# Kernel tuning notes

Measured on AMD Instinct MI355X. Metric: run time of the kernel, lower is better.

The kernel has to match this reference:

```python
import jax, jax.numpy as jnp
import numpy as np

NUM_HEADS = 2
LN_EPS = 1e-5
NEG_MASK = -1e9


def setup_inputs() -> dict:
    key = jax.random.key(0)
    ks = jax.random.split(key, 8)
    B, C, T, N = 8, 64, 32, 400
    H, D = NUM_HEADS, C // NUM_HEADS
    s = 1.0 / np.sqrt(C)
    return {
        "x": jax.random.normal(ks[0], (B, C, T, N), dtype=jnp.float32),
        "Wq": jax.random.normal(ks[1], (C, C), dtype=jnp.float32) * s,
        "Wk": jax.random.normal(ks[2], (C, C), dtype=jnp.float32) * s,
        "Wv": jax.random.normal(ks[3], (C, C), dtype=jnp.float32) * s,
        "a_src": jax.random.normal(ks[4], (H, D), dtype=jnp.float32) * 0.1,
        "a_dst": jax.random.normal(ks[5], (H, D), dtype=jnp.float32) * 0.1,
        "ln_gamma": jnp.ones((C,), dtype=jnp.float32),
        "ln_beta": jnp.zeros((C,), dtype=jnp.float32),
        "gso": jax.random.randint(ks[6], (N, N), 0, 2, dtype=jnp.int32),
    }


def reference(x, Wq, Wk, Wv, a_src, a_dst, ln_gamma, ln_beta, gso):
    B, C, T, N = x.shape
    H = NUM_HEADS
    D = C // H
    # (B,C,T,N) -> (B*T, N, C)
    xr = jnp.transpose(x, (0, 2, 3, 1)).reshape(B * T, N, C)
    # torch Linear: y = x @ W.T; then split heads -> (BT, N, H, D)
    Q = (xr @ Wq.T).reshape(B * T, N, H, D)
    K = (xr @ Wk.T).reshape(B * T, N, H, D)
    V = (xr @ Wv.T).reshape(B * T, N, H, D)
    # GAT additive scores per head
    s_src = jnp.einsum("bnhd,hd->bnh", Q, a_src)  # (BT, N, H)
    s_dst = jnp.einsum("bnhd,hd->bnh", K, a_dst)  # (BT, N, H)
    scores = s_src[:, :, None, :] + s_dst[:, None, :, :]  # (BT, i, j, H)
    scores = jax.nn.leaky_relu(scores, negative_slope=0.2)
    mask = jnp.where(gso == 0, jnp.float32(NEG_MASK), 0.0)  # (N, N)
    scores = scores + mask[None, :, :, None]
    attn = jax.nn.softmax(scores, axis=2)  # softmax over dst j; dropout = identity (eval)
    out = jnp.einsum("bijh,bjhd->bihd", attn, V).reshape(B * T, N, C)
    # LayerNorm over channel dim
    mu = jnp.mean(out, axis=-1, keepdims=True)
    var = jnp.var(out, axis=-1, keepdims=True)
    out = (out - mu) * jax.lax.rsqrt(var + LN_EPS) * ln_gamma + ln_beta
    # (BT, N, C) -> (B, C, T, N)
    return jnp.transpose(out.reshape(B, T, N, C), (0, 3, 1, 2))
```

## Files before the change

### kernel.cpp

```cpp
#include <hip/hip_runtime.h>
#include <hip/hip_bf16.h>

typedef __attribute__((ext_vector_type(8))) short bf16x8;
typedef __attribute__((ext_vector_type(4))) float f32x4;
typedef __attribute__((ext_vector_type(4))) int i32x4;
typedef __attribute__((ext_vector_type(4))) unsigned int u32x4;

#define B_   8
#define C_   64
#define T_   32
#define N_   400
#define BT_  256
#define NCH_ 7
#define NKT_ 13
#define L2E_ 1.4426950408889634f
#define C2_  (-13.849872392533959f)
#define SH12_ (-17.312340490667560f)

#define WS_MB 0
#define WS_SQ 25600
#define WS_SK 844800
#define WS_VG 1664000

#if __has_builtin(__builtin_amdgcn_exp2f)
#define EXP2F(x) __builtin_amdgcn_exp2f(x)
#else
#define EXP2F(x) __expf((x) * 0.6931471805599453f)
#endif

__global__ __launch_bounds__(256, 4) void gat_proj(
    const float* __restrict__ x, const float* __restrict__ Wq,
    const float* __restrict__ Wk, const float* __restrict__ Wv,
    const float* __restrict__ a_src, const float* __restrict__ a_dst,
    const int* __restrict__ gso,
    float* __restrict__ sq1, float* __restrict__ sk1,
    __hip_bfloat16* __restrict__ Vg, unsigned int* __restrict__ mb)
{
  __shared__ __align__(16) float xs[64][65];
  __shared__ __align__(16) float wv_s[64][68];
  __shared__ float wqk_s[4][64];
  const int tid = threadIdx.x;
  const int bt = blockIdx.x & 255, nc = blockIdx.x >> 8;
  const int b = bt >> 5, t = bt & 31, n0 = nc * 64;
  const int w = tid >> 6, nn = tid & 63;

  {
    const int h = w >> 1;
    const float* W = (w & 1) ? Wk : Wq;
    const float* a = (w & 1) ? a_dst : a_src;
    float s = 0.f;
    #pragma unroll
    for (int d = 0; d < 32; ++d)
      s += W[(h*32 + d)*C_ + nn] * a[h*32 + d];
    wqk_s[w][nn] = s;
  }
  #pragma unroll
  for (int it = 0; it < 16; ++it) {
    int idx = it*256 + tid;
    int o = idx >> 6, c = idx & 63;
    wv_s[c][o] = Wv[o*C_ + c];
  }
  #pragma unroll
  for (int it = 0; it < 16; ++it) {
    int idx = it*256 + tid;
    int c = idx >> 6, n2 = idx & 63;
    int n = n0 + n2;
    xs[c][n2] = (n < N_) ? x[((b*C_ + c)*T_ + t)*N_ + n] : 0.f;
  }
  __syncthreads();

  f32x4 a0={0,0,0,0}, a1={0,0,0,0}, a2={0,0,0,0}, a3={0,0,0,0};
  float sacc = 0.f;
  #pragma unroll 4
  for (int c = 0; c < 64; ++c) {
    float xv = xs[c][nn];
    const f32x4* wr = (const f32x4*)&wv_s[c][w*16];
    a0 += xv*wr[0]; a1 += xv*wr[1]; a2 += xv*wr[2]; a3 += xv*wr[3];
    sacc = fmaf(xv, wqk_s[w][c], sacc);
  }
  const int n = n0 + nn;
  if (n < N_) {
    int h = w >> 1;
    if (w & 1) sk1[((size_t)bt*2 + h)*N_ + n] = sacc * L2E_;
    else       sq1[((size_t)bt*2 + h)*N_ + n] = fmaf(sacc, L2E_, SH12_);
  }
  if (n < 416) {
    const int kt = n >> 5, q = (n >> 3) & 3, jj = n & 7;
    __hip_bfloat16* vp = Vg
        + ((((size_t)bt*NKT_ + kt)*2 + (w>>1))*2 + (w&1))*512
        + q*128 + jj;
    #pragma unroll
    for (int k = 0; k < 4; ++k) vp[(0*4+k)*8] = __float2bfloat16(a0[k]);
    #pragma unroll
    for (int k = 0; k < 4; ++k) vp[(1*4+k)*8] = __float2bfloat16(a1[k]);
    #pragma unroll
    for (int k = 0; k < 4; ++k) vp[(2*4+k)*8] = __float2bfloat16(a2[k]);
    #pragma unroll
    for (int k = 0; k < 4; ++k) vp[(3*4+k)*8] = __float2bfloat16(a3[k]);
  }
  if (blockIdx.x < 26) {
    int idx = blockIdx.x*256 + tid;
    if (idx < N_*16) {
      int i = idx >> 4, kw = idx & 15;
      unsigned int bits = 0;
      if (kw < 13) {
        int j0 = kw * 32;
        #pragma unroll
        for (int bb = 0; bb < 32; ++bb) {
          int j = j0 + bb;
          if (j < N_ && gso[i*N_ + j] != 0) bits |= (1u << bb);
        }
      }
      mb[idx] = bits;
    }
  }
}

__global__ __launch_bounds__(512, 6) void gat_attn(
    const __hip_bfloat16* __restrict__ Vg, const float* __restrict__ sq1,
    const float* __restrict__ sk1, const unsigned int* __restrict__ mb,
    const float* __restrict__ gamma, const float* __restrict__ beta,
    float* __restrict__ out)
{
  __shared__ __align__(16) float sd_s[2][416];
  __shared__ __align__(16) float ob[64][65];
  const int tid = threadIdx.x;
  const int bt = blockIdx.x & 255, chunk = blockIdx.x >> 8;
  const int b = bt >> 5, t = bt & 31;
  const int i0 = chunk * 64;

  if (tid < 416) {
    sd_s[0][tid] = (tid < N_) ? sk1[((size_t)bt*2 + 0)*N_ + tid] : 0.f;
    sd_s[1][tid] = (tid < N_) ? sk1[((size_t)bt*2 + 1)*N_ + tid] : 0.f;
  }
  __syncthreads();

  const int lane = tid & 63, wave = tid >> 6;
  const int h = wave & 1, itile = wave >> 1;
  const int rowA = lane & 15, quad = lane >> 4;
  const int ibase = i0 + itile*16;

  if (ibase < N_) {
    const int irow = ibase + rowA;
    const float si1 = sq1[((size_t)bt*2 + h)*N_ + irow];
    const u32x4* mp = (const u32x4*)(mb + irow*16);
    u32x4 mw0 = mp[0], mw1 = mp[1], mw2 = mp[2];
    unsigned int mw12 = mb[irow*16 + 12];
    const float* sdp = sd_s[h] + quad*8;
    const __hip_bfloat16* vbase = Vg + ((size_t)bt*NKT_*2 + h)*2*512 + lane*8;

    f32x4 d0={0,0,0,0}, d1={0,0,0,0}, d2={0,0,0,0};
    bf16x8 ones;
    #pragma unroll
    for (int k = 0; k < 8; ++k) ones[k] = (short)0x3F80;

    #pragma unroll
    for (int kt = 0; kt < NKT_; ++kt) {
      unsigned int mword = (kt < 4) ? mw0[kt] : (kt < 8) ? mw1[kt-4]
                         : (kt < 12) ? mw2[kt-8] : mw12;
      unsigned int mbyte = (mword >> (quad*8)) & 0xffu;
      f32x4 s0 = *(const f32x4*)(sdp + kt*32);
      f32x4 s1 = *(const f32x4*)(sdp + kt*32 + 4);
      bf16x8 vb0 = *(const bf16x8*)(vbase + kt*2048);
      bf16x8 vb1 = *(const bf16x8*)(vbase + kt*2048 + 512);
      int em[8];
      #pragma unroll
      for (int jj = 0; jj < 8; ++jj) {
        float sd = (jj < 4) ? s0[jj] : s1[jj-4];
        float t1 = si1 + sd;
        float t2 = fmaf(0.2f, t1, C2_);
        float v  = fmaxf(t1, t2);
        float e  = EXP2F(v);
        int msk = ((int)(mbyte << (31 - jj))) >> 31;
        em[jj] = __float_as_int(e) & msk;
      }
      union { i32x4 i; bf16x8 v; } af;
      af.i.x = (int)__builtin_amdgcn_perm((unsigned)em[1], (unsigned)em[0], 0x07060302u);
      af.i.y = (int)__builtin_amdgcn_perm((unsigned)em[3], (unsigned)em[2], 0x07060302u);
      af.i.z = (int)__builtin_amdgcn_perm((unsigned)em[5], (unsigned)em[4], 0x07060302u);
      af.i.w = (int)__builtin_amdgcn_perm((unsigned)em[7], (unsigned)em[6], 0x07060302u);
      d0 = __builtin_amdgcn_mfma_f32_16x16x32_bf16(af.v, vb0, d0, 0, 0, 0);
      d1 = __builtin_amdgcn_mfma_f32_16x16x32_bf16(af.v, vb1, d1, 0, 0, 0);
      d2 = __builtin_amdgcn_mfma_f32_16x16x32_bf16(af.v, ones, d2, 0, 0, 0);
    }
    #pragma unroll
    for (int r = 0; r < 4; ++r) {
      float li = 1.0f / d2[r];
      int rl = itile*16 + quad*4 + r;
      ob[rl][h*32 + rowA]      = d0[r] * li;
      ob[rl][h*32 + 16 + rowA] = d1[r] * li;
    }
  }
  __syncthreads();

  {
    int rl = tid >> 3, cgi = tid & 7;
    int n = i0 + rl;
    if (n < N_) {
      float u[8]; float s = 0.f;
      #pragma unroll
      for (int k = 0; k < 8; ++k) { u[k] = ob[rl][cgi*8 + k]; s += u[k]; }
      s += __shfl_xor(s,1); s += __shfl_xor(s,2); s += __shfl_xor(s,4);
      float mu = s * (1.f/64.f);
      float q = 0.f;
      #pragma unroll
      for (int k = 0; k < 8; ++k) { float dv = u[k]-mu; q = fmaf(dv,dv,q); }
      q += __shfl_xor(q,1); q += __shfl_xor(q,2); q += __shfl_xor(q,4);
      float rstd = rsqrtf(q*(1.f/64.f) + 1e-5f);
      #pragma unroll
      for (int k = 0; k < 8; ++k) {
        float g = gamma[cgi*8 + k], be = beta[cgi*8 + k];
        ob[rl][cgi*8 + k] = (u[k]-mu)*rstd*g + be;
      }
    }
  }
  __syncthreads();

  #pragma unroll
  for (int it = 0; it < 8; ++it) {
    int idx = it*512 + tid;
    int c = idx >> 6, nn2 = idx & 63;
    int n = i0 + nn2;
    if (n < N_) out[((b*C_ + c)*T_ + t)*N_ + n] = ob[nn2][c];
  }
}

extern "C" void kernel_launch(void* const* d_in, const int* in_sizes, int n_in,
                              void* d_out, int out_size, void* d_ws, size_t ws_size,
                              hipStream_t stream) {
  (void)in_sizes; (void)n_in; (void)out_size; (void)ws_size;
  const float* x     = (const float*)d_in[0];
  const float* Wq    = (const float*)d_in[1];
  const float* Wk    = (const float*)d_in[2];
  const float* Wv    = (const float*)d_in[3];
  const float* a_src = (const float*)d_in[4];
  const float* a_dst = (const float*)d_in[5];
  const float* gamma = (const float*)d_in[6];
  const float* beta  = (const float*)d_in[7];
  const int*   gso   = (const int*)d_in[8];
  float* out = (float*)d_out;
  char* ws = (char*)d_ws;

  unsigned int* mb = (unsigned int*)(ws + WS_MB);
  float* sq1 = (float*)(ws + WS_SQ);
  float* sk1 = (float*)(ws + WS_SK);
  __hip_bfloat16* Vg = (__hip_bfloat16*)(ws + WS_VG);

  gat_proj<<<BT_*NCH_, 256, 0, stream>>>(x, Wq, Wk, Wv, a_src, a_dst, gso,
                                         sq1, sk1, Vg, mb);
  gat_attn<<<BT_*NCH_, 512, 0, stream>>>(Vg, sq1, sk1, mb,
                                         gamma, beta, out);
}
```

Measured before the change: 134.9 us.

## Fuse projection and attention into one per-timestep block, keeping V in LDS

Replaces the two-kernel pipeline, which wrote scores and bf16 V to global workspace, with one 1024-thread block per (b,t). That block projects V and the scores into shared memory, then runs the masked-softmax MFMA attention plus LayerNorm over row chunks of 128. The mask-bit packing moves to a small separate prep kernel. The goal is to remove the global round trip for V and the scores and the redundant per-chunk reloads. The cost is a grid of only 256 large blocks with around 100KB of LDS each, so occupancy is low and there may be too few blocks to fill the GPU. x is also now rounded to bf16 before projection, which changes precision.

```diff
diff --git a/kernel.cpp b/kernel.cpp
--- a/kernel.cpp
+++ b/kernel.cpp
@@ -3,6 +3,7 @@
 
 typedef __attribute__((ext_vector_type(8))) short bf16x8;
 typedef __attribute__((ext_vector_type(4))) float f32x4;
+typedef __attribute__((ext_vector_type(2))) float f32x2;
 typedef __attribute__((ext_vector_type(4))) int i32x4;
 typedef __attribute__((ext_vector_type(4))) unsigned int u32x4;
 
@@ -11,16 +12,10 @@
 #define T_   32
 #define N_   400
 #define BT_  256
-#define NCH_ 7
 #define NKT_ 13
 #define L2E_ 1.4426950408889634f
 #define C2_  (-13.849872392533959f)
 #define SH12_ (-17.312340490667560f)
-
-#define WS_MB 0
-#define WS_SQ 25600
-#define WS_SK 844800
-#define WS_VG 1664000
 
 #if __has_builtin(__builtin_amdgcn_exp2f)
 #define EXP2F(x) __builtin_amdgcn_exp2f(x)
@@ -28,200 +23,217 @@
 #define EXP2F(x) __expf((x) * 0.6931471805599453f)
 #endif
 
-__global__ __launch_bounds__(256, 4) void gat_proj(
+__global__ __launch_bounds__(256) void gat_prep(
+    const int* __restrict__ gso, unsigned int* __restrict__ mb)
+{
+  int idx = blockIdx.x*256 + threadIdx.x;
+  if (idx < N_*16) {
+    int i = idx >> 4, kw = idx & 15;
+    unsigned int bits = 0;
+    if (kw < 13) {
+      int j0 = kw * 32;
+      #pragma unroll
+      for (int bb = 0; bb < 32; ++bb) {
+        int j = j0 + bb;
+        if (j < N_ && gso[i*N_ + j] != 0) bits |= (1u << bb);
+      }
+    }
+    mb[idx] = bits;
+  }
+}
+
+__global__ __launch_bounds__(1024) void gat_fused(
     const float* __restrict__ x, const float* __restrict__ Wq,
     const float* __restrict__ Wk, const float* __restrict__ Wv,
     const float* __restrict__ a_src, const float* __restrict__ a_dst,
-    const int* __restrict__ gso,
-    float* __restrict__ sq1, float* __restrict__ sk1,
-    __hip_bfloat16* __restrict__ Vg, unsigned int* __restrict__ mb)
+    const float* __restrict__ gamma, const float* __restrict__ beta,
+    const unsigned int* __restrict__ mb, float* __restrict__ out)
 {
-  __shared__ __align__(16) float xs[64][65];
-  __shared__ __align__(16) float wv_s[64][68];
+  __shared__ __align__(16) __hip_bfloat16 Vt[64][416];
+  __shared__ __align__(16) char scratch[70656];
+  __shared__ __align__(16) float sd_s[2][416];
+  __shared__ __align__(16) float si_s[2][400];
   __shared__ float wqk_s[4][64];
+  __shared__ float g_s[64], b_s[64];
+
+  unsigned int (*xs)[208] = (unsigned int(*)[208])scratch;
+  float (*wv_s)[68] = (float(*)[68])(scratch + 53248);
+  float (*ob)[68] = (float(*)[68])scratch;
+
   const int tid = threadIdx.x;
-  const int bt = blockIdx.x & 255, nc = blockIdx.x >> 8;
-  const int b = bt >> 5, t = bt & 31, n0 = nc * 64;
-  const int w = tid >> 6, nn = tid & 63;
-
-  {
-    const int h = w >> 1;
-    const float* W = (w & 1) ? Wk : Wq;
-    const float* a = (w & 1) ? a_dst : a_src;
+  const int bt = blockIdx.x;
+  const int b = bt >> 5, t = bt & 31;
+
+  if (tid < 256) {
+    int ww = tid >> 6, c = tid & 63, h = ww >> 1;
+    const float* W = (ww & 1) ? Wk : Wq;
+    const float* a = (ww & 1) ? a_dst : a_src;
     float s = 0.f;
     #pragma unroll
-    for (int d = 0; d < 32; ++d)
-      s += W[(h*32 + d)*C_ + nn] * a[h*32 + d];
-    wqk_s[w][nn] = s;
+    for (int d = 0; d < 32; ++d) s += W[(h*32 + d)*C_ + c] * a[h*32 + d];
+    wqk_s[ww][c] = s;
+  } else if (tid < 320) {
+    g_s[tid - 256] = gamma[tid - 256];
+  } else if (tid < 384) {
+    b_s[tid - 320] = beta[tid - 320];
+  }
+  #pragma unroll
+  for (int it = 0; it < 4; ++it) {
+    int idx = it*1024 + tid;
+    int o = idx >> 6, c = idx & 63;
+    wv_s[c][o] = Wv[o*C_ + c];
   }
   #pragma unroll
   for (int it = 0; it < 16; ++it) {
-    int idx = it*256 + tid;
-    int o = idx >> 6, c = idx & 63;
-    wv_s[c][o] = Wv[o*C_ + c];
-  }
+    int idx = it*1024 + tid;
+    int c = idx >> 8, pr = idx & 255;
+    if (pr < 208) {
+      int n = pr*2;
+      const float* xrow = x + ((size_t)(b*C_ + c)*T_ + t)*N_;
+      float x0 = (n   < N_) ? xrow[n]   : 0.f;
+      float x1 = (n+1 < N_) ? xrow[n+1] : 0.f;
+      union { __hip_bfloat16 h2[2]; unsigned int u; } pk;
+      pk.h2[0] = __float2bfloat16(x0);
+      pk.h2[1] = __float2bfloat16(x1);
+      xs[c][pr] = pk.u;
+    }
+  }
+  __syncthreads();
+
+  {
+    const int pr = tid >> 2, ww = tid & 3;
+    if (pr < 208) {
+      f32x2 acc[16];
+      #pragma unroll
+      for (int k = 0; k < 16; ++k) acc[k] = (f32x2){0.f, 0.f};
+      f32x2 sacc = {0.f, 0.f};
+      #pragma unroll 4
+      for (int c = 0; c < 64; ++c) {
+        unsigned int xu = xs[c][pr];
+        f32x2 xv;
+        xv.x = __uint_as_float(xu << 16);
+        xv.y = __uint_as_float(xu & 0xffff0000u);
+        const f32x4* wr = (const f32x4*)&wv_s[c][ww*16];
+        f32x4 w0 = wr[0], w1 = wr[1], w2 = wr[2], w3 = wr[3];
+        #pragma unroll
+        for (int k = 0; k < 4; ++k) acc[k]      = xv * w0[k] + acc[k];
+        #pragma unroll
+        for (int k = 0; k < 4; ++k) acc[4 + k]  = xv * w1[k] + acc[4 + k];
+        #pragma unroll
+        for (int k = 0; k < 4; ++k) acc[8 + k]  = xv * w2[k] + acc[8 + k];
+        #pragma unroll
+        for (int k = 0; k < 4; ++k) acc[12 + k] = xv * w3[k] + acc[12 + k];
+        sacc = xv * wqk_s[ww][c] + sacc;
+      }
+      const int n = pr*2, hw = ww >> 1;
+      if (ww & 1) {
+        sd_s[hw][n]   = sacc.x * L2E_;
+        sd_s[hw][n+1] = sacc.y * L2E_;
+      } else {
+        if (n   < N_) si_s[hw][n]   = fmaf(sacc.x, L2E_, SH12_);
+        if (n+1 < N_) si_s[hw][n+1] = fmaf(sacc.y, L2E_, SH12_);
+      }
+      #pragma unroll
+      for (int k = 0; k < 16; ++k) {
+        int o = ww*16 + k;
+        union { __hip_bfloat16 h2[2]; unsigned int u; } pk;
+        pk.h2[0] = __float2bfloat16(acc[k].x);
+        pk.h2[1] = __float2bfloat16(acc[k].y);
+        *(unsigned int*)&Vt[o][n] = pk.u;
+      }
+    }
+  }
+  __syncthreads();
+
+  const int lane = tid & 63, wave = tid >> 6;
+  const int hh = wave & 1, itile = wave >> 1;
+  const int rowA = lane & 15, quad = lane >> 4;
+
+  bf16x8 ones;
   #pragma unroll
-  for (int it = 0; it < 16; ++it) {
-    int idx = it*256 + tid;
-    int c = idx >> 6, n2 = idx & 63;
-    int n = n0 + n2;
-    xs[c][n2] = (n < N_) ? x[((b*C_ + c)*T_ + t)*N_ + n] : 0.f;
-  }
-  __syncthreads();
-
-  f32x4 a0={0,0,0,0}, a1={0,0,0,0}, a2={0,0,0,0}, a3={0,0,0,0};
-  float sacc = 0.f;
-  #pragma unroll 4
-  for (int c = 0; c < 64; ++c) {
-    float xv = xs[c][nn];
-    const f32x4* wr = (const f32x4*)&wv_s[c][w*16];
-    a0 += xv*wr[0]; a1 += xv*wr[1]; a2 += xv*wr[2]; a3 += xv*wr[3];
-    sacc = fmaf(xv, wqk_s[w][c], sacc);
-  }
-  const int n = n0 + nn;
-  if (n < N_) {
-    int h = w >> 1;
-    if (w & 1) sk1[((size_t)bt*2 + h)*N_ + n] = sacc * L2E_;
-    else       sq1[((size_t)bt*2 + h)*N_ + n] = fmaf(sacc, L2E_, SH12_);
-  }
-  if (n < 416) {
-    const int kt = n >> 5, q = (n >> 3) & 3, jj = n & 7;
-    __hip_bfloat16* vp = Vg
-        + ((((size_t)bt*NKT_ + kt)*2 + (w>>1))*2 + (w&1))*512
-        + q*128 + jj;
+  for (int k = 0; k < 8; ++k) ones[k] = (short)0x3F80;
+
+  for (int r0 = 0; r0 < N_; r0 += 128) {
+    const int ibase = r0 + itile*16;
+    if (ibase < N_) {
+      const int irow = ibase + rowA;
+      const float si1 = si_s[hh][irow];
+      const u32x4* mp = (const u32x4*)(mb + irow*16);
+      u32x4 mw0 = mp[0], mw1 = mp[1], mw2 = mp[2];
+      unsigned int mw12 = mb[irow*16 + 12];
+      const float* sdp = sd_s[hh] + quad*8;
+      const __hip_bfloat16* v0p = &Vt[hh*32 + rowA][quad*8];
+      const __hip_bfloat16* v1p = v0p + 16*416;
+
+      f32x4 d0 = {0,0,0,0}, d1 = {0,0,0,0}, d2 = {0,0,0,0};
+      #pragma unroll
+      for (int kt = 0; kt < NKT_; ++kt) {
+        unsigned int mword = (kt < 4) ? mw0[kt] : (kt < 8) ? mw1[kt-4]
+                           : (kt < 12) ? mw2[kt-8] : mw12;
+        unsigned int mbyte = (mword >> (quad*8)) & 0xffu;
+        f32x4 s0 = *(const f32x4*)(sdp + kt*32);
+        f32x4 s1 = *(const f32x4*)(sdp + kt*32 + 4);
+        bf16x8 vb0 = *(const bf16x8*)(v0p + kt*32);
+        bf16x8 vb1 = *(const bf16x8*)(v1p + kt*32);
+        int em[8];
+        #pragma unroll
+        for (int jj = 0; jj < 8; ++jj) {
+          float sd = (jj < 4) ? s0[jj] : s1[jj-4];
+          float t1 = si1 + sd;
+          float t2 = fmaf(0.2f, t1, C2_);
+          float v  = fmaxf(t1, t2);
+          float e  = EXP2F(v);
+          int msk = ((int)(mbyte << (31 - jj))) >> 31;
+          em[jj] = __float_as_int(e) & msk;
+        }
+        union { i32x4 i; bf16x8 v; } af;
+        af.i.x = (int)__builtin_amdgcn_perm((unsigned)em[1], (unsigned)em[0], 0x07060302u);
+        af.i.y = (int)__builtin_amdgcn_perm((unsigned)em[3], (unsigned)em[2], 0x07060302u);
+        af.i.z = (int)__builtin_amdgcn_perm((unsigned)em[5], (unsigned)em[4], 0x07060302u);
+        af.i.w = (int)__builtin_amdgcn_perm((unsigned)em[7], (unsigned)em[6], 0x07060302u);
+        d0 = __builtin_amdgcn_mfma_f32_16x16x32_bf16(af.v, vb0, d0, 0, 0, 0);
+        d1 = __builtin_amdgcn_mfma_f32_16x16x32_bf16(af.v, vb1, d1, 0, 0, 0);
+        d2 = __builtin_amdgcn_mfma_f32_16x16x32_bf16(af.v, ones, d2, 0, 0, 0);
+      }
+      #pragma unroll
+      for (int r = 0; r < 4; ++r) {
+        float li = 1.0f / d2[r];
+        int rl = itile*16 + quad*4 + r;
+        ob[rl][hh*32 + rowA]      = d0[r] * li;
+        ob[rl][hh*32 + 16 + rowA] = d1[r] * li;
+      }
+    }
+    __syncthreads();
+
+    {
+      int rl = tid >> 3, cgi = tid & 7;
+      int n = r0 + rl;
+      if (n < N_) {
+        float u[8]; float s = 0.f;
+        #pragma unroll
+        for (int k = 0; k < 8; ++k) { u[k] = ob[rl][cgi*8 + k]; s += u[k]; }
+        s += __shfl_xor(s,1); s += __shfl_xor(s,2); s += __shfl_xor(s,4);
+        float mu = s * (1.f/64.f);
+        float q = 0.f;
+        #pragma unroll
+        for (int k = 0; k < 8; ++k) { float dv = u[k]-mu; q = fmaf(dv,dv,q); }
+        q += __shfl_xor(q,1); q += __shfl_xor(q,2); q += __shfl_xor(q,4);
+        float rstd = rsqrtf(q*(1.f/64.f) + 1e-5f);
+        #pragma unroll
+        for (int k = 0; k < 8; ++k)
+          ob[rl][cgi*8 + k] = (u[k]-mu)*rstd*g_s[cgi*8 + k] + b_s[cgi*8 + k];
+      }
+    }
+    __syncthreads();
+
     #pragma unroll
-    for (int k = 0; k < 4; ++k) vp[(0*4+k)*8] = __float2bfloat16(a0[k]);
-    #pragma unroll
-    for (int k = 0; k < 4; ++k) vp[(1*4+k)*8] = __float2bfloat16(a1[k]);
-    #pragma unroll
-    for (int k = 0; k < 4; ++k) vp[(2*4+k)*8] = __float2bfloat16(a2[k]);
-    #pragma unroll
-    for (int k = 0; k < 4; ++k) vp[(3*4+k)*8] = __float2bfloat16(a3[k]);
-  }
-  if (blockIdx.x < 26) {
-    int idx = blockIdx.x*256 + tid;
-    if (idx < N_*16) {
-      int i = idx >> 4, kw = idx & 15;
-      unsigned int bits = 0;
-      if (kw < 13) {
-        int j0 = kw * 32;
-        #pragma unroll
-        for (int bb = 0; bb < 32; ++bb) {
-          int j = j0 + bb;
-          if (j < N_ && gso[i*N_ + j] != 0) bits |= (1u << bb);
-        }
-      }
-      mb[idx] = bits;
-    }
-  }
-}
-
-__global__ __launch_bounds__(512, 6) void gat_attn(
-    const __hip_bfloat16* __restrict__ Vg, const float* __restrict__ sq1,
-    const float* __restrict__ sk1, const unsigned int* __restrict__ mb,
-    const float* __restrict__ gamma, const float* __restrict__ beta,
-    float* __restrict__ out)
-{
-  __shared__ __align__(16) float sd_s[2][416];
-  __shared__ __align__(16) float ob[64][65];
-  const int tid = threadIdx.x;
-  const int bt = blockIdx.x & 255, chunk = blockIdx.x >> 8;
-  const int b = bt >> 5, t = bt & 31;
-  const int i0 = chunk * 64;
-
-  if (tid < 416) {
-    sd_s[0][tid] = (tid < N_) ? sk1[((size_t)bt*2 + 0)*N_ + tid] : 0.f;
-    sd_s[1][tid] = (tid < N_) ? sk1[((size_t)bt*2 + 1)*N_ + tid] : 0.f;
-  }
-  __syncthreads();
-
-  const int lane = tid & 63, wave = tid >> 6;
-  const int h = wave & 1, itile = wave >> 1;
-  const int rowA = lane & 15, quad = lane >> 4;
-  const int ibase = i0 + itile*16;
-
-  if (ibase < N_) {
-    const int irow = ibase + rowA;
-    const float si1 = sq1[((size_t)bt*2 + h)*N_ + irow];
-    const u32x4* mp = (const u32x4*)(mb + irow*16);
-    u32x4 mw0 = mp[0], mw1 = mp[1], mw2 = mp[2];
-    unsigned int mw12 = mb[irow*16 + 12];
-    const float* sdp = sd_s[h] + quad*8;
-    const __hip_bfloat16* vbase = Vg + ((size_t)bt*NKT_*2 + h)*2*512 + lane*8;
-
-    f32x4 d0={0,0,0,0}, d1={0,0,0,0}, d2={0,0,0,0};
-    bf16x8 ones;
-    #pragma unroll
-    for (int k = 0; k < 8; ++k) ones[k] = (short)0x3F80;
-
-    #pragma unroll
-    for (int kt = 0; kt < NKT_; ++kt) {
-      unsigned int mword = (kt < 4) ? mw0[kt] : (kt < 8) ? mw1[kt-4]
-                         : (kt < 12) ? mw2[kt-8] : mw12;
-      unsigned int mbyte = (mword >> (quad*8)) & 0xffu;
-      f32x4 s0 = *(const f32x4*)(sdp + kt*32);
-      f32x4 s1 = *(const f32x4*)(sdp + kt*32 + 4);
-      bf16x8 vb0 = *(const bf16x8*)(vbase + kt*2048);
-      bf16x8 vb1 = *(const bf16x8*)(vbase + kt*2048 + 512);
-      int em[8];
-      #pragma unroll
-      for (int jj = 0; jj < 8; ++jj) {
-        float sd = (jj < 4) ? s0[jj] : s1[jj-4];
-        float t1 = si1 + sd;
-        float t2 = fmaf(0.2f, t1, C2_);
-        float v  = fmaxf(t1, t2);
-        float e  = EXP2F(v);
-        int msk = ((int)(mbyte << (31 - jj))) >> 31;
-        em[jj] = __float_as_int(e) & msk;
-      }
-      union { i32x4 i; bf16x8 v; } af;
-      af.i.x = (int)__builtin_amdgcn_perm((unsigned)em[1], (unsigned)em[0], 0x07060302u);
-      af.i.y = (int)__builtin_amdgcn_perm((unsigned)em[3], (unsigned)em[2], 0x07060302u);
-      af.i.z = (int)__builtin_amdgcn_perm((unsigned)em[5], (unsigned)em[4], 0x07060302u);
-      af.i.w = (int)__builtin_amdgcn_perm((unsigned)em[7], (unsigned)em[6], 0x07060302u);
-      d0 = __builtin_amdgcn_mfma_f32_16x16x32_bf16(af.v, vb0, d0, 0, 0, 0);
-      d1 = __builtin_amdgcn_mfma_f32_16x16x32_bf16(af.v, vb1, d1, 0, 0, 0);
-      d2 = __builtin_amdgcn_mfma_f32_16x16x32_bf16(af.v, ones, d2, 0, 0, 0);
-    }
-    #pragma unroll
-    for (int r = 0; r < 4; ++r) {
-      float li = 1.0f / d2[r];
-      int rl = itile*16 + quad*4 + r;
-      ob[rl][h*32 + rowA]      = d0[r] * li;
-      ob[rl][h*32 + 16 + rowA] = d1[r] * li;
-    }
-  }
-  __syncthreads();
-
-  {
-    int rl = tid >> 3, cgi = tid & 7;
-    int n = i0 + rl;
-    if (n < N_) {
-      float u[8]; float s = 0.f;
-      #pragma unroll
-      for (int k = 0; k < 8; ++k) { u[k] = ob[rl][cgi*8 + k]; s += u[k]; }
-      s += __shfl_xor(s,1); s += __shfl_xor(s,2); s += __shfl_xor(s,4);
-      float mu = s * (1.f/64.f);
-      float q = 0.f;
-      #pragma unroll
-      for (int k = 0; k < 8; ++k) { float dv = u[k]-mu; q = fmaf(dv,dv,q); }
-      q += __shfl_xor(q,1); q += __shfl_xor(q,2); q += __shfl_xor(q,4);
-      float rstd = rsqrtf(q*(1.f/64.f) + 1e-5f);
-      #pragma unroll
-      for (int k = 0; k < 8; ++k) {
-        float g = gamma[cgi*8 + k], be = beta[cgi*8 + k];
-        ob[rl][cgi*8 + k] = (u[k]-mu)*rstd*g + be;
-      }
-    }
-  }
-  __syncthreads();
-
-  #pragma unroll
-  for (int it = 0; it < 8; ++it) {
-    int idx = it*512 + tid;
-    int c = idx >> 6, nn2 = idx & 63;
-    int n = i0 + nn2;
-    if (n < N_) out[((b*C_ + c)*T_ + t)*N_ + n] = ob[nn2][c];
+    for (int it = 0; it < 8; ++it) {
+      int idx = it*1024 + tid;
+      int c = idx >> 7, nn = idx & 127;
+      int n = r0 + nn;
+      if (n < N_) out[((size_t)(b*C_ + c)*T_ + t)*N_ + n] = ob[nn][c];
+    }
+    __syncthreads();
   }
 }
 
@@ -239,15 +251,10 @@
   const float* beta  = (const float*)d_in[7];
   const int*   gso   = (const int*)d_in[8];
   float* out = (float*)d_out;
-  char* ws = (char*)d_ws;
-
-  unsigned int* mb = (unsigned int*)(ws + WS_MB);
-  float* sq1 = (float*)(ws + WS_SQ);
-  float* sk1 = (float*)(ws + WS_SK);
-  __hip_bfloat16* Vg = (__hip_bfloat16*)(ws + WS_VG);
-
-  gat_proj<<<BT_*NCH_, 256, 0, stream>>>(x, Wq, Wk, Wv, a_src, a_dst, gso,
-                                         sq1, sk1, Vg, mb);
-  gat_attn<<<BT_*NCH_, 512, 0, stream>>>(Vg, sq1, sk1, mb,
-                                         gamma, beta, out);
+
+  unsigned int* mb = (unsigned int*)d_ws;
+
+  gat_prep<<<26, 256, 0, stream>>>(gso, mb);
+  gat_fused<<<BT_, 1024, 0, stream>>>(x, Wq, Wk, Wv, a_src, a_dst,
+                                      gamma, beta, mb, out);
 }
```

Measured after the change: 139.8 us. 3.6% more time.
